# Kernel tuning notes

Measured on AMD Instinct MI355X. Metric: run time of the kernel, lower is better.

## Reference

```python
import jax, jax.numpy as jnp
import numpy as np


def setup_inputs() -> dict:
    key = jax.random.key(0)
    ks = jax.random.split(key, 8)
    B = 32768
    return {
        "x": jax.random.normal(ks[0], (B, 784), dtype=jnp.float32),
        "conv_w": jax.random.normal(ks[1], (3, 3), dtype=jnp.float32),
        "fc1_w": jax.random.normal(ks[2], (512, 676), dtype=jnp.float32) * 0.04,
        "fc1_b": jax.random.normal(ks[3], (512,), dtype=jnp.float32),
        "fc2_w": jax.random.normal(ks[4], (512, 512), dtype=jnp.float32) * 0.04,
        "fc2_b": jax.random.normal(ks[5], (512,), dtype=jnp.float32),
        "out_w": jax.random.normal(ks[6], (10, 512), dtype=jnp.float32) * 0.04,
        "out_b": jax.random.normal(ks[7], (10,), dtype=jnp.float32),
    }


def reference(x, conv_w, fc1_w, fc1_b, fc2_w, fc2_b, out_w, out_b):
    B = x.shape[0]
    img = x.reshape(B, 1, 28, 28)  # NCHW, single channel
    # Valid 3x3 cross-correlation (same math as the nested tensordot loop).
    kern = conv_w.reshape(1, 1, 3, 3)  # OIHW
    conv = jax.lax.conv_general_dilated(
        img, kern, window_strides=(1, 1), padding="VALID",
        dimension_numbers=("NCHW", "OIHW", "NCHW"))  # [B,1,26,26]
    h = conv.reshape(B, 26 * 26)
    h = jax.nn.relu(h @ fc1_w.T + fc1_b)
    h = jax.nn.relu(h @ fc2_w.T + fc2_b)
    return h @ out_w.T + out_b  # [B,10] logits
```

## Files before the change

kernel.cpp:

```cpp
#include <hip/hip_runtime.h>

typedef unsigned short ushort_t;
typedef __attribute__((ext_vector_type(8))) short bf16x8;
typedef __attribute__((ext_vector_type(4))) float f32x4;
typedef __attribute__((ext_vector_type(16))) float f32x16;

__device__ __forceinline__ unsigned short f2bf(float f) {
    union { float f; unsigned u; } v; v.f = f;
    unsigned r = v.u + 0x7FFFu + ((v.u >> 16) & 1u);
    return (unsigned short)(r >> 16);
}

__global__ __launch_bounds__(256) void prep_w(const float* __restrict__ fc1_w,
                                              const float* __restrict__ cw,
                                              const float* __restrict__ fc2_w,
                                              const float* __restrict__ out_w,
                                              ushort_t* __restrict__ W1,
                                              ushort_t* __restrict__ W2,
                                              ushort_t* __restrict__ W3) {
    const int idx = blockIdx.x * 256 + threadIdx.x;
    if (idx < 425984) {
        const int ngrp = idx / 26624;
        const int kfrag = (idx % 26624) >> 9;
        const int li = idx & 511;
        const int lane = li >> 3, e = li & 7;
        const int n = ngrp * 32 + (lane & 31);
        const int p = kfrag * 16 + (lane >> 5) * 8 + e;
        float acc = 0.f;
        if (p < 784) {
            const int pr = p / 28, pc = p % 28;
#pragma unroll
            for (int dr = 0; dr < 3; ++dr) {
                const int r = pr - dr;
                if (r < 0 || r >= 26) continue;
#pragma unroll
                for (int dc = 0; dc < 3; ++dc) {
                    const int col = pc - dc;
                    if (col < 0 || col >= 26) continue;
                    acc += cw[dr * 3 + dc] * fc1_w[n * 676 + r * 26 + col];
                }
            }
        }
        W1[idx] = f2bf(acc);
    }
    if (idx < 262144) {
        const int ngrp = idx / 16384;
        const int kfrag = (idx % 16384) >> 9;
        const int li = idx & 511;
        const int lane = li >> 3, e = li & 7;
        const int n = ngrp * 32 + (lane & 31);
        const int p = kfrag * 16 + (lane >> 5) * 8 + e;
        W2[idx] = f2bf(fc2_w[n * 512 + p]);
    }
    if (idx < 16 * 512)  W3[idx] = (idx < 10 * 512) ? f2bf(out_w[idx]) : (ushort_t)0;
}

__global__ __launch_bounds__(1024, 4) void mega4(const float* __restrict__ x,
                                                 const ushort_t* __restrict__ W1,
                                                 const ushort_t* __restrict__ W2,
                                                 const ushort_t* __restrict__ W3,
                                                 const float* __restrict__ b1,
                                                 const float* __restrict__ b2,
                                                 const float* __restrict__ ob,
                                                 float* __restrict__ out) {
    extern __shared__ ushort_t smem[];
    ushort_t* xs0 = smem;
    ushort_t* hs  = smem + 8192;

    const int tid = threadIdx.x;
    const int wave = tid >> 6, lane = tid & 63;
    const int r32 = lane & 31, khalf = lane >> 5;
    const int xrow = tid >> 3, xoct = tid & 7;
    const int m0 = blockIdx.x * 128;

    f32x16 acc[2][2];
#pragma unroll
    for (int a = 0; a < 2; ++a)
#pragma unroll
        for (int i = 0; i < 2; ++i)
#pragma unroll
            for (int e = 0; e < 16; ++e) acc[a][i][e] = 0.f;

    f32x4 xv0, xv1;
    auto load_x = [&](int ks) {
        const int gc = ks * 64 + xoct * 8;
        if (gc < 784) {
            const f32x4* p = (const f32x4*)&x[(size_t)(m0 + xrow) * 784 + gc];
            xv0 = __builtin_nontemporal_load(p);
            xv1 = __builtin_nontemporal_load(p + 1);
        } else {
            xv0 = (f32x4){0.f, 0.f, 0.f, 0.f};
            xv1 = (f32x4){0.f, 0.f, 0.f, 0.f};
        }
    };
    auto store_x = [&](ushort_t* buf) {
        bf16x8 xv;
        xv[0] = (short)f2bf(xv0.x); xv[1] = (short)f2bf(xv0.y);
        xv[2] = (short)f2bf(xv0.z); xv[3] = (short)f2bf(xv0.w);
        xv[4] = (short)f2bf(xv1.x); xv[5] = (short)f2bf(xv1.y);
        xv[6] = (short)f2bf(xv1.z); xv[7] = (short)f2bf(xv1.w);
        *(bf16x8*)&buf[xrow * 64 + ((xoct ^ (xrow & 7)) * 8)] = xv;
    };

    load_x(0);
    store_x(xs0);
    __syncthreads();

    for (int ks = 0; ks < 13; ++ks) {
        if (ks < 12) load_x(ks + 1);
        const ushort_t* bufp = (ks & 1) ? hs : xs0;
#pragma unroll
        for (int ksub = 0; ksub < 4; ++ksub) {
            const int kfrag = ks * 4 + ksub;
            const bf16x8 bw = *(const bf16x8*)&W1[((size_t)wave * 52 + kfrag) * 512 + lane * 8];
            const int q = 2 * ksub + khalf;
            bf16x8 af[2][2];
#pragma unroll
            for (int mh = 0; mh < 2; ++mh)
#pragma unroll
                for (int i = 0; i < 2; ++i) {
                    const int mr = mh * 64 + i * 32 + r32;
                    af[mh][i] = *(const bf16x8*)&bufp[mr * 64 + ((q ^ (mr & 7)) * 8)];
                }
#pragma unroll
            for (int mh = 0; mh < 2; ++mh)
#pragma unroll
                for (int i = 0; i < 2; ++i)
                    acc[mh][i] = __builtin_amdgcn_mfma_f32_32x32x16_bf16(af[mh][i], bw, acc[mh][i], 0, 0, 0);
        }
        if (ks < 12) {
            store_x((ks & 1) ? xs0 : hs);
            __syncthreads();
        }
    }
    __syncthreads();

    {
        const int n = wave * 32 + r32;
        const float bb = b1[n];
        const int nseg = n >> 3, nrem = n & 7;
#pragma unroll
        for (int mh = 0; mh < 2; ++mh)
#pragma unroll
            for (int i = 0; i < 2; ++i)
#pragma unroll
                for (int reg = 0; reg < 16; ++reg) {
                    const int m = mh * 64 + i * 32 + 4 * khalf + (reg & 3) + 8 * (reg >> 2);
                    hs[m * 512 + ((nseg ^ (m & 7)) * 8) + nrem] = f2bf(fmaxf(acc[mh][i][reg] + bb, 0.f));
                }
    }
#pragma unroll
    for (int a = 0; a < 2; ++a)
#pragma unroll
        for (int i = 0; i < 2; ++i)
#pragma unroll
            for (int e = 0; e < 16; ++e) acc[a][i][e] = 0.f;
    __syncthreads();

    for (int ks = 0; ks < 8; ++ks) {
#pragma unroll
        for (int ksub = 0; ksub < 4; ++ksub) {
            const int kfrag = ks * 4 + ksub;
            const bf16x8 bw = *(const bf16x8*)&W2[((size_t)wave * 32 + kfrag) * 512 + lane * 8];
            const int hq = ks * 8 + 2 * ksub + khalf;
            bf16x8 af[2][2];
#pragma unroll
            for (int mh = 0; mh < 2; ++mh)
#pragma unroll
                for (int i = 0; i < 2; ++i) {
                    const int m = mh * 64 + i * 32 + r32;
                    af[mh][i] = *(const bf16x8*)&hs[m * 512 + ((hq ^ (m & 7)) * 8)];
                }
#pragma unroll
            for (int mh = 0; mh < 2; ++mh)
#pragma unroll
                for (int i = 0; i < 2; ++i)
                    acc[mh][i] = __builtin_amdgcn_mfma_f32_32x32x16_bf16(af[mh][i], bw, acc[mh][i], 0, 0, 0);
        }
    }
    __syncthreads();

    {
        const int n = wave * 32 + r32;
        const float bb = b2[n];
        const int nseg = n >> 3, nrem = n & 7;
#pragma unroll
        for (int mh = 0; mh < 2; ++mh)
#pragma unroll
            for (int i = 0; i < 2; ++i)
#pragma unroll
                for (int reg = 0; reg < 16; ++reg) {
                    const int m = mh * 64 + i * 32 + 4 * khalf + (reg & 3) + 8 * (reg >> 2);
                    hs[m * 512 + ((nseg ^ (m & 7)) * 8) + nrem] = f2bf(fmaxf(acc[mh][i][reg] + bb, 0.f));
                }
    }
    __syncthreads();

    if (wave < 8) {
        const int quad = lane >> 4, l16 = lane & 15;
        const int row = wave * 16 + l16;
        f32x4 hacc = {0.f, 0.f, 0.f, 0.f};
#pragma unroll
        for (int ks = 0; ks < 16; ++ks) {
            const int seg = 4 * ks + quad;
            const bf16x8 a = *(const bf16x8*)&hs[row * 512 + ((seg ^ (row & 7)) * 8)];
            const bf16x8 b = *(const bf16x8*)&W3[l16 * 512 + ks * 32 + quad * 8];
            hacc = __builtin_amdgcn_mfma_f32_16x16x32_bf16(a, b, hacc, 0, 0, 0);
        }
        if (l16 < 10) {
            const float bb = ob[l16];
#pragma unroll
            for (int r = 0; r < 4; ++r)
                out[(size_t)(m0 + wave * 16 + quad * 4 + r) * 10 + l16] = hacc[r] + bb;
        }
    }
}

extern "C" void kernel_launch(void* const* d_in, const int* in_sizes, int n_in,
                              void* d_out, int out_size, void* d_ws, size_t ws_size,
                              hipStream_t stream) {
    const float* x      = (const float*)d_in[0];
    const float* conv_w = (const float*)d_in[1];
    const float* fc1_w  = (const float*)d_in[2];
    const float* fc1_b  = (const float*)d_in[3];
    const float* fc2_w  = (const float*)d_in[4];
    const float* fc2_b  = (const float*)d_in[5];
    const float* out_w  = (const float*)d_in[6];
    const float* out_b  = (const float*)d_in[7];
    float* out = (float*)d_out;

    ushort_t* W1 = (ushort_t*)d_ws;
    ushort_t* W2 = W1 + 425984;
    ushort_t* W3 = W2 + 262144;

    prep_w<<<dim3(1664), 256, 0, stream>>>(fc1_w, conv_w, fc2_w, out_w, W1, W2, W3);

    mega4<<<dim3(256), 1024, 147456, stream>>>(x, W1, W2, W3, fc1_b, fc2_b, out_b, out);
}
```

Baseline: 215.8 us.

## Halve block row tile and give each wave two output column groups

Each block now handles 64 rows with 512 threads instead of 128 rows with 1024 threads. Every wave computes a 2x2 tile of MFMA outputs over two 32-column groups, which cuts repeated LDS activation reads. The last fc1 k-step is peeled out of the loop, and the MFMA bursts are wrapped in s_setprio. Shared memory per block is halved, so two blocks can be resident on one CU and their phases can overlap. In exchange, weight fragments are re-read from L2 twice as often per row.

```diff
diff --git a/kernel.cpp b/kernel.cpp
--- a/kernel.cpp
+++ b/kernel.cpp
@@ -55,31 +55,32 @@
     if (idx < 16 * 512)  W3[idx] = (idx < 10 * 512) ? f2bf(out_w[idx]) : (ushort_t)0;
 }
 
-__global__ __launch_bounds__(1024, 4) void mega4(const float* __restrict__ x,
-                                                 const ushort_t* __restrict__ W1,
-                                                 const ushort_t* __restrict__ W2,
-                                                 const ushort_t* __restrict__ W3,
-                                                 const float* __restrict__ b1,
-                                                 const float* __restrict__ b2,
-                                                 const float* __restrict__ ob,
-                                                 float* __restrict__ out) {
+__global__ __launch_bounds__(512, 4) void mega5(const float* __restrict__ x,
+                                                const ushort_t* __restrict__ W1,
+                                                const ushort_t* __restrict__ W2,
+                                                const ushort_t* __restrict__ W3,
+                                                const float* __restrict__ b1,
+                                                const float* __restrict__ b2,
+                                                const float* __restrict__ ob,
+                                                float* __restrict__ out) {
     extern __shared__ ushort_t smem[];
     ushort_t* xs0 = smem;
-    ushort_t* hs  = smem + 8192;
+    ushort_t* hs  = smem + 4096;
 
     const int tid = threadIdx.x;
     const int wave = tid >> 6, lane = tid & 63;
     const int r32 = lane & 31, khalf = lane >> 5;
     const int xrow = tid >> 3, xoct = tid & 7;
-    const int m0 = blockIdx.x * 128;
+    const int m0 = blockIdx.x * 64;
+    const size_t ng0 = wave * 2, ng1 = wave * 2 + 1;
 
     f32x16 acc[2][2];
 #pragma unroll
     for (int a = 0; a < 2; ++a)
 #pragma unroll
-        for (int i = 0; i < 2; ++i)
-#pragma unroll
-            for (int e = 0; e < 16; ++e) acc[a][i][e] = 0.f;
+        for (int j = 0; j < 2; ++j)
+#pragma unroll
+            for (int e = 0; e < 16; ++e) acc[a][j][e] = 0.f;
 
     f32x4 xv0, xv1;
     auto load_x = [&](int ks) {
@@ -102,101 +103,107 @@
         *(bf16x8*)&buf[xrow * 64 + ((xoct ^ (xrow & 7)) * 8)] = xv;
     };
 
+    auto write_h = [&](const float* __restrict__ bias) {
+#pragma unroll
+        for (int j = 0; j < 2; ++j) {
+            const int n = (wave * 2 + j) * 32 + r32;
+            const float bb = bias[n];
+            const int nseg = n >> 3, nrem = n & 7;
+#pragma unroll
+            for (int i = 0; i < 2; ++i)
+#pragma unroll
+                for (int reg = 0; reg < 16; ++reg) {
+                    const int m = i * 32 + 4 * khalf + (reg & 3) + 8 * (reg >> 2);
+                    hs[m * 512 + ((nseg ^ (m & 7)) * 8) + nrem] = f2bf(fmaxf(acc[i][j][reg] + bb, 0.f));
+                }
+        }
+    };
+
     load_x(0);
     store_x(xs0);
     __syncthreads();
 
-    for (int ks = 0; ks < 13; ++ks) {
-        if (ks < 12) load_x(ks + 1);
+    for (int ks = 0; ks < 12; ++ks) {
+        load_x(ks + 1);
         const ushort_t* bufp = (ks & 1) ? hs : xs0;
 #pragma unroll
         for (int ksub = 0; ksub < 4; ++ksub) {
             const int kfrag = ks * 4 + ksub;
-            const bf16x8 bw = *(const bf16x8*)&W1[((size_t)wave * 52 + kfrag) * 512 + lane * 8];
+            const bf16x8 bw0 = *(const bf16x8*)&W1[(ng0 * 52 + kfrag) * 512 + lane * 8];
+            const bf16x8 bw1 = *(const bf16x8*)&W1[(ng1 * 52 + kfrag) * 512 + lane * 8];
             const int q = 2 * ksub + khalf;
-            bf16x8 af[2][2];
-#pragma unroll
-            for (int mh = 0; mh < 2; ++mh)
-#pragma unroll
-                for (int i = 0; i < 2; ++i) {
-                    const int mr = mh * 64 + i * 32 + r32;
-                    af[mh][i] = *(const bf16x8*)&bufp[mr * 64 + ((q ^ (mr & 7)) * 8)];
-                }
-#pragma unroll
-            for (int mh = 0; mh < 2; ++mh)
-#pragma unroll
-                for (int i = 0; i < 2; ++i)
-                    acc[mh][i] = __builtin_amdgcn_mfma_f32_32x32x16_bf16(af[mh][i], bw, acc[mh][i], 0, 0, 0);
-        }
-        if (ks < 12) {
-            store_x((ks & 1) ? xs0 : hs);
-            __syncthreads();
-        }
-    }
-    __syncthreads();
-
+            bf16x8 af[2];
+#pragma unroll
+            for (int i = 0; i < 2; ++i) {
+                const int m = i * 32 + r32;
+                af[i] = *(const bf16x8*)&bufp[m * 64 + ((q ^ (m & 7)) * 8)];
+            }
+            __builtin_amdgcn_s_setprio(1);
+            acc[0][0] = __builtin_amdgcn_mfma_f32_32x32x16_bf16(af[0], bw0, acc[0][0], 0, 0, 0);
+            acc[0][1] = __builtin_amdgcn_mfma_f32_32x32x16_bf16(af[0], bw1, acc[0][1], 0, 0, 0);
+            acc[1][0] = __builtin_amdgcn_mfma_f32_32x32x16_bf16(af[1], bw0, acc[1][0], 0, 0, 0);
+            acc[1][1] = __builtin_amdgcn_mfma_f32_32x32x16_bf16(af[1], bw1, acc[1][1], 0, 0, 0);
+            __builtin_amdgcn_s_setprio(0);
+        }
+        store_x((ks & 1) ? xs0 : hs);
+        __syncthreads();
+    }
     {
-        const int n = wave * 32 + r32;
-        const float bb = b1[n];
-        const int nseg = n >> 3, nrem = n & 7;
-#pragma unroll
-        for (int mh = 0; mh < 2; ++mh)
-#pragma unroll
-            for (int i = 0; i < 2; ++i)
-#pragma unroll
-                for (int reg = 0; reg < 16; ++reg) {
-                    const int m = mh * 64 + i * 32 + 4 * khalf + (reg & 3) + 8 * (reg >> 2);
-                    hs[m * 512 + ((nseg ^ (m & 7)) * 8) + nrem] = f2bf(fmaxf(acc[mh][i][reg] + bb, 0.f));
-                }
-    }
+        const ushort_t* bufp = xs0;
+        const int kfrag = 48;
+        const bf16x8 bw0 = *(const bf16x8*)&W1[(ng0 * 52 + kfrag) * 512 + lane * 8];
+        const bf16x8 bw1 = *(const bf16x8*)&W1[(ng1 * 52 + kfrag) * 512 + lane * 8];
+        const int q = khalf;
+        bf16x8 af[2];
+#pragma unroll
+        for (int i = 0; i < 2; ++i) {
+            const int m = i * 32 + r32;
+            af[i] = *(const bf16x8*)&bufp[m * 64 + ((q ^ (m & 7)) * 8)];
+        }
+        __builtin_amdgcn_s_setprio(1);
+        acc[0][0] = __builtin_amdgcn_mfma_f32_32x32x16_bf16(af[0], bw0, acc[0][0], 0, 0, 0);
+        acc[0][1] = __builtin_amdgcn_mfma_f32_32x32x16_bf16(af[0], bw1, acc[0][1], 0, 0, 0);
+        acc[1][0] = __builtin_amdgcn_mfma_f32_32x32x16_bf16(af[1], bw0, acc[1][0], 0, 0, 0);
+        acc[1][1] = __builtin_amdgcn_mfma_f32_32x32x16_bf16(af[1], bw1, acc[1][1], 0, 0, 0);
+        __builtin_amdgcn_s_setprio(0);
+    }
+
+    write_h(b1);
 #pragma unroll
     for (int a = 0; a < 2; ++a)
 #pragma unroll
-        for (int i = 0; i < 2; ++i)
-#pragma unroll
-            for (int e = 0; e < 16; ++e) acc[a][i][e] = 0.f;
+        for (int j = 0; j < 2; ++j)
+#pragma unroll
+            for (int e = 0; e < 16; ++e) acc[a][j][e] = 0.f;
     __syncthreads();
 
     for (int ks = 0; ks < 8; ++ks) {
 #pragma unroll
         for (int ksub = 0; ksub < 4; ++ksub) {
             const int kfrag = ks * 4 + ksub;
-            const bf16x8 bw = *(const bf16x8*)&W2[((size_t)wave * 32 + kfrag) * 512 + lane * 8];
+            const bf16x8 bw0 = *(const bf16x8*)&W2[(ng0 * 32 + kfrag) * 512 + lane * 8];
+            const bf16x8 bw1 = *(const bf16x8*)&W2[(ng1 * 32 + kfrag) * 512 + lane * 8];
             const int hq = ks * 8 + 2 * ksub + khalf;
-            bf16x8 af[2][2];
-#pragma unroll
-            for (int mh = 0; mh < 2; ++mh)
-#pragma unroll
-                for (int i = 0; i < 2; ++i) {
-                    const int m = mh * 64 + i * 32 + r32;
-                    af[mh][i] = *(const bf16x8*)&hs[m * 512 + ((hq ^ (m & 7)) * 8)];
-                }
-#pragma unroll
-            for (int mh = 0; mh < 2; ++mh)
-#pragma unroll
-                for (int i = 0; i < 2; ++i)
-                    acc[mh][i] = __builtin_amdgcn_mfma_f32_32x32x16_bf16(af[mh][i], bw, acc[mh][i], 0, 0, 0);
-        }
-    }
-    __syncthreads();
-
-    {
-        const int n = wave * 32 + r32;
-        const float bb = b2[n];
-        const int nseg = n >> 3, nrem = n & 7;
-#pragma unroll
-        for (int mh = 0; mh < 2; ++mh)
-#pragma unroll
-            for (int i = 0; i < 2; ++i)
-#pragma unroll
-                for (int reg = 0; reg < 16; ++reg) {
-                    const int m = mh * 64 + i * 32 + 4 * khalf + (reg & 3) + 8 * (reg >> 2);
-                    hs[m * 512 + ((nseg ^ (m & 7)) * 8) + nrem] = f2bf(fmaxf(acc[mh][i][reg] + bb, 0.f));
-                }
-    }
-    __syncthreads();
-
-    if (wave < 8) {
+            bf16x8 af[2];
+#pragma unroll
+            for (int i = 0; i < 2; ++i) {
+                const int m = i * 32 + r32;
+                af[i] = *(const bf16x8*)&hs[m * 512 + ((hq ^ (m & 7)) * 8)];
+            }
+            __builtin_amdgcn_s_setprio(1);
+            acc[0][0] = __builtin_amdgcn_mfma_f32_32x32x16_bf16(af[0], bw0, acc[0][0], 0, 0, 0);
+            acc[0][1] = __builtin_amdgcn_mfma_f32_32x32x16_bf16(af[0], bw1, acc[0][1], 0, 0, 0);
+            acc[1][0] = __builtin_amdgcn_mfma_f32_32x32x16_bf16(af[1], bw0, acc[1][0], 0, 0, 0);
+            acc[1][1] = __builtin_amdgcn_mfma_f32_32x32x16_bf16(af[1], bw1, acc[1][1], 0, 0, 0);
+            __builtin_amdgcn_s_setprio(0);
+        }
+    }
+    __syncthreads();
+
+    write_h(b2);
+    __syncthreads();
+
+    if (wave < 4) {
         const int quad = lane >> 4, l16 = lane & 15;
         const int row = wave * 16 + l16;
         f32x4 hacc = {0.f, 0.f, 0.f, 0.f};
@@ -235,5 +242,5 @@
 
     prep_w<<<dim3(1664), 256, 0, stream>>>(fc1_w, conv_w, fc2_w, out_w, W1, W2, W3);
 
-    mega4<<<dim3(256), 1024, 147456, stream>>>(x, W1, W2, W3, fc1_b, fc2_b, out_b, out);
-}
+    mega5<<<dim3(512), 512, 73728, stream>>>(x, W1, W2, W3, fc1_b, fc2_b, out_b, out);
+}
```

Measured after the change: 216.8 us. No clear change (+0.5%).
